# Optimization experiments

Hardware: AMD Instinct MI355X
Metric: run time of the kernel (lower is better)

## Reference

```python
import jax, jax.numpy as jnp
import numpy as np

HEAD_NUM = 16

def setup_inputs() -> dict:
    key = jax.random.key(0)
    k1, k2 = jax.random.split(key)
    bs, seq, d = 2, 2048, 1024
    embeddings = jax.random.normal(k1, (bs, seq, d), dtype=jnp.float32)
    W = jax.random.normal(k2, (d, 3 * d), dtype=jnp.float32) * (1.0 / np.sqrt(d))
    b = jnp.zeros((3 * d,), dtype=jnp.float32)
    return {"embeddings": embeddings, "W": W, "b": b}

def reference(embeddings, W, b):
    bs, seq, d = embeddings.shape
    h = HEAD_NUM
    qkv = embeddings @ W + b                      # [b, s, 3d]
    q, k, v = jnp.split(qkv, 3, axis=-1)          # each [b, s, d]
    hd = d // h
    # Faithful to source: reshape to (bs, seq, head_dim, heads) then permute
    def split_heads(x, head_dim):
        return x.reshape(bs, seq, head_dim, h).transpose(0, 3, 1, 2)  # [b, h, s, hd]
    mq = split_heads(q, hd)
    mk = split_heads(k, hd)
    mv = split_heads(v, hd)
    scale = jnp.sqrt(jnp.asarray(hd, dtype=mq.dtype))
    scores = jnp.einsum('bhqd,bhkd->bhqk', mq, mk) / scale  # [b, h, s, s]
    attn = jax.nn.softmax(scores, axis=-1)
    out = jnp.einsum('bhqk,bhkv->bhqv', attn, mv)            # [b, h, s, hd]
    return out.transpose(0, 2, 1, 3).reshape(bs, seq, -1)    # [b, s, d]
```

## Files before the change

### kernel.cpp

```cpp
#include <hip/hip_runtime.h>
#include <stdint.h>

typedef unsigned short u16;
typedef unsigned int u32;
typedef unsigned int u32x2 __attribute__((ext_vector_type(2)));
typedef float f32x4 __attribute__((ext_vector_type(4)));
typedef __bf16 bf16x8 __attribute__((ext_vector_type(8)));

#define BS 2
#define SEQ 2048
#define DIM 1024
#define NW3 3072
#define NH 16
#define HD 64

#define MFMA_BF16(a, b, c) __builtin_amdgcn_mfma_f32_16x16x32_bf16((a), (b), (c), 0, 0, 0)

#define GLL16(g, l)                                                                \
  __builtin_amdgcn_global_load_lds(                                                \
      (__attribute__((address_space(1))) void*)(void*)(uintptr_t)(g),              \
      (__attribute__((address_space(3))) void*)(l), 16, 0, 0)

__device__ __forceinline__ float fexp2(float x) {
#if defined(__has_builtin)
#if __has_builtin(__builtin_amdgcn_exp2f)
  return __builtin_amdgcn_exp2f(x);
#else
  return exp2f(x);
#endif
#else
  return exp2f(x);
#endif
}

__device__ __forceinline__ u16 f2bf(float x) {
  __bf16 h = (__bf16)x;
  return __builtin_bit_cast(u16, h);
}

#define CSC 0.18033688011112042f

#if defined(__has_builtin)
#if __has_builtin(__builtin_amdgcn_permlane32_swap) && \
    __has_builtin(__builtin_amdgcn_permlane16_swap)
#define HAVE_PLSWAP 1
#endif
#endif

__device__ __forceinline__ uint4 p_transform(u32 pk00, u32 pk01, u32 pk10, u32 pk11,
                                             int sl0, int sl1, bool hi) {
#ifdef HAVE_PLSWAP
  u32x2 s0 = __builtin_amdgcn_permlane32_swap(pk00, pk10, false, false);
  u32x2 s1 = __builtin_amdgcn_permlane32_swap(pk01, pk11, false, false);
  u32x2 t0 = __builtin_amdgcn_permlane16_swap(s0[0], s0[1], false, false);
  u32x2 t1 = __builtin_amdgcn_permlane16_swap(s1[0], s1[1], false, false);
  uint4 wv;
  wv.x = t0[0]; wv.y = t1[0]; wv.z = t0[1]; wv.w = t1[1];
  return wv;
#else
  u32 a0 = __shfl(pk00, sl0), a1 = __shfl(pk01, sl0);
  u32 a2 = __shfl(pk00, sl1), a3 = __shfl(pk01, sl1);
  u32 b0 = __shfl(pk10, sl0), b1 = __shfl(pk11, sl0);
  u32 b2 = __shfl(pk10, sl1), b3 = __shfl(pk11, sl1);
  uint4 wv;
  wv.x = hi ? b0 : a0; wv.y = hi ? b1 : a1;
  wv.z = hi ? b2 : a2; wv.w = hi ? b3 : a3;
  return wv;
#endif
}

__global__ __launch_bounds__(256) void conv_kernel(const float* __restrict__ A,
                                                   u16* __restrict__ O,
                                                   const float* __restrict__ W,
                                                   u16* __restrict__ Wt) {
  if (blockIdx.x < 4096) {
    int i = (blockIdx.x * 256 + threadIdx.x) * 4;
    float4 v = *(const float4*)(A + i);
    union { u16 u[4]; ushort4 v4; } p;
    p.u[0] = f2bf(v.x); p.u[1] = f2bf(v.y); p.u[2] = f2bf(v.z); p.u[3] = f2bf(v.w);
    *(ushort4*)(O + i) = p.v4;
  } else {
    __shared__ __align__(16) u16 lt[64][68];
    int b2 = blockIdx.x - 4096;
    int ktile = b2 / 48, ntile = b2 - ktile * 48;
    int k0 = ktile * 64, n0 = ntile * 64;
    int rowb = threadIdx.x >> 4, c4 = (threadIdx.x & 15) * 4;
#pragma unroll
    for (int rr = 0; rr < 4; ++rr) {
      int row = rowb + rr * 16;
      float4 v = *(const float4*)(W + (size_t)(k0 + row) * NW3 + n0 + c4);
      union { u16 u[4]; uint2 d; } pk;
      pk.u[0] = f2bf(v.x); pk.u[1] = f2bf(v.y); pk.u[2] = f2bf(v.z); pk.u[3] = f2bf(v.w);
      *(uint2*)&lt[row][c4] = pk.d;
    }
    __syncthreads();
    int j = threadIdx.x >> 2, seg = threadIdx.x & 3;
    int n = n0 + j;
    int h = n & 15, hd = (n & 1023) >> 4;
    int np = (n & ~1023) + h * 64 + hd;
    union { u16 u[16]; uint4 q[2]; } o;
#pragma unroll
    for (int idx = 0; idx < 16; ++idx) o.u[idx] = lt[seg * 16 + idx][j];
    u16* dst = Wt + (size_t)np * DIM + k0 + seg * 16;
    *(uint4*)(dst) = o.q[0];
    *(uint4*)(dst + 8) = o.q[1];
  }
}

#define GSTAGE(ADST, BDST, KT)                                                 \
  {                                                                            \
    const int koff = (KT) * 64;                                \
    _Pragma("unroll") for (int r = 0; r < 2; ++r) {                            \
      int l = r * 256 + t;                            \
      int row = l >> 2, pos = l & 3;                                           \
      int kc = pos ^ (row & 3);                                                \
      GLL16(Abase + row * 2048 + koff + kc * 16, (char*)(ADST) + l * 16);      \
      GLL16(Bbase + row * 2048 + koff + kc * 16, (char*)(BDST) + l * 16);      \
    }                                                                          \
  }

#define GCOMPUTE(AT, BT)                                                       \
  {                                                                            \
    bf16x8 af[4], bfr[4];                                                      \
    _Pragma("unroll") for (int mt = 0; mt < 4; ++mt) {                         \
      int row = wm + mt * 16 + c;                                              \
      int kc = quad ^ (row & 3);                                               \
      af[mt] = *(const bf16x8*)((const char*)(AT) + row * 64 + kc * 16);       \
    }                                                                          \
    _Pragma("unroll") for (int nt = 0; nt < 4; ++nt) {                         \
      int row = wn + nt * 16 + c;                                              \
      int kc = quad ^ (row & 3);                                               \
      bfr[nt] = *(const bf16x8*)((const char*)(BT) + row * 64 + kc * 16);      \
    }                                                                          \
    _Pragma("unroll") for (int mt = 0; mt < 4; ++mt)                           \
      _Pragma("unroll") for (int nt = 0; nt < 4; ++nt)                         \
        acc[mt][nt] = MFMA_BF16(af[mt], bfr[nt], acc[mt][nt]);                 \
  }

__global__ __launch_bounds__(256) void gemm_qkv_kernel(
    const u16* __restrict__ Ab, const u16* __restrict__ Bt, const float* __restrict__ bias,
    u16* __restrict__ Q, u16* __restrict__ K, u16* __restrict__ Vt) {
  __shared__ __align__(16) u16 A0[128 * 32];
  __shared__ __align__(16) u16 A1[128 * 32];
  __shared__ __align__(16) u16 A2[128 * 32];
  __shared__ __align__(16) u16 B0[128 * 32];
  __shared__ __align__(16) u16 B1[128 * 32];
  __shared__ __align__(16) u16 B2[128 * 32];
  const int t = threadIdx.x;
  const int lane = t & 63, wave = t >> 6;
  const int c = lane & 15, quad = lane >> 4;
  const int wid = (blockIdx.x & 7) * 96 + (blockIdx.x >> 3);
  const int tm = wid / 24, tn = wid - tm * 24;
  const int wm = (wave >> 1) * 64, wn = (wave & 1) * 64;

  const char* Abase = (const char*)(Ab + (size_t)tm * 128 * DIM);
  const char* Bbase = (const char*)(Bt + (size_t)tn * 128 * DIM);

  f32x4 z = {0.f, 0.f, 0.f, 0.f};
  f32x4 acc[4][4];
#pragma unroll
  for (int i = 0; i < 4; ++i)
#pragma unroll
    for (int j = 0; j < 4; ++j) acc[i][j] = z;

  GSTAGE(A0, B0, 0);
  GSTAGE(A1, B1, 1);
  asm volatile("s_waitcnt vmcnt(4)" ::: "memory");
  __builtin_amdgcn_s_barrier();
  __builtin_amdgcn_sched_barrier(0);

  const u16 *pa = A0, *pb = B0;
  const u16 *qa = A1, *qb = B1;
  const u16 *ra = A2, *rb = B2;
#pragma unroll 1
  for (int kt = 0; kt < 32; ++kt) {
    if (kt + 2 < 32) GSTAGE(ra, rb, kt + 2);
    GCOMPUTE(pa, pb);
    if (kt + 2 < 32) {
      asm volatile("s_waitcnt vmcnt(4)" ::: "memory");
    } else {
      asm volatile("s_waitcnt vmcnt(0)" ::: "memory");
    }
    __builtin_amdgcn_s_barrier();
    __builtin_amdgcn_sched_barrier(0);
    const u16* ta = pa; pa = qa; qa = ra; ra = ta;
    const u16* tb = pb; pb = qb; qb = rb; rb = tb;
  }

#pragma unroll
  for (int nt = 0; nt < 4; ++nt) {
    int np = tn * 128 + wn + nt * 16 + c;
    int which = np >> 10;
    int rem = np & 1023;
    int h = rem >> 6, hd = rem & 63;
    float bv = bias[(np & ~1023) + hd * 16 + h];
    float sc = (which == 0) ? CSC : 1.0f;
    float bvs = bv * sc;
#pragma unroll
    for (int mt = 0; mt < 4; ++mt) {
      int mbase = tm * 128 + wm + mt * 16 + quad * 4;
      int bI = mbase >> 11;
      int s0 = mbase & 2047;
      if (which == 2) {
        union { u16 u[4]; uint2 v; } p;
#pragma unroll
        for (int r = 0; r < 4; ++r) p.u[r] = f2bf(acc[mt][nt][r] + bv);
        *(uint2*)(Vt + ((size_t)(bI * NH + h) * HD + hd) * SEQ + s0) = p.v;
      } else {
        u16* dst = (which == 0) ? Q : K;
#pragma unroll
        for (int r = 0; r < 4; ++r)
          dst[((size_t)(bI * NH + h) * SEQ + (s0 + r)) * HD + hd] =
              f2bf(acc[mt][nt][r] * sc + bvs);
      }
    }
  }
}

#define STAGE_KV(KDST, VDST, KTILE)                                            \
  {                                                                            \
    const char* Ktb = Kb + (size_t)(KTILE) * 8192;        \
    const char* Vtb = Vb + (size_t)(KTILE) * 128;         \
    _Pragma("unroll") for (int r = 0; r < 2; ++r) {                            \
      int l = r * 256 + t;                                                     \
      int row = l >> 3, pos = l & 7;                                           \
      int kc = pos ^ (row & 7);                                                \
      GLL16(Ktb + row * 128 + kc * 16, (char*)(KDST) + l * 16);                \
      GLL16(Vtb + row * 4096 + kc * 16, (char*)(VDST) + l * 16);               \
    }                                                                          \
  }

#define COMPUTE_TILE(KT, VT)                                                   \
  {                                                                            \
    f32x4 sT[2][2]; \
    sT[0][0] = z; sT[0][1] = z; sT[1][0] = z; sT[1][1] = z;                    \
    __builtin_amdgcn_s_setprio(1);                                             \
    _Pragma("unroll") for (int mt2 = 0; mt2 < 2; ++mt2) {                      \
      _Pragma("unroll") for (int ks = 0; ks < 2; ++ks) {                       \
        int row = ws * 32 + mt2 * 16 + c;                                      \
        int kc = (ks * 4 + quad) ^ (row & 7);                                  \
        bf16x8 kf = *(const bf16x8*)((const char*)(KT) + row * 128 + kc * 16); \
        sT[mt2][0] = MFMA_BF16(kf, qf[0][ks], sT[mt2][0]);                     \
        sT[mt2][1] = MFMA_BF16(kf, qf[1][ks], sT[mt2][1]);                     \
      }                                                                        \
    }                                                                          \
    __builtin_amdgcn_s_setprio(0);                                             \
    bf16x8 pf[2];                                                              \
    _Pragma("unroll") for (int nt = 0; nt < 2; ++nt) {                         \
      u32 pk[2][2];                                                            \
      _Pragma("unroll") for (int mt2 = 0; mt2 < 2; ++mt2) {                    \
        float p0 = fexp2(sT[mt2][nt][0]);                                      \
        float p1 = fexp2(sT[mt2][nt][1]);                                      \
        float p2 = fexp2(sT[mt2][nt][2]);                                      \
        float p3 = fexp2(sT[mt2][nt][3]);                                      \
        pk[mt2][0] = (u32)f2bf(p0) | ((u32)f2bf(p1) << 16);                    \
        pk[mt2][1] = (u32)f2bf(p2) | ((u32)f2bf(p3) << 16);                    \
      }                                                                        \
      uint4 wv = p_transform(pk[0][0], pk[0][1], pk[1][0], pk[1][1],           \
                             sl0, sl1, hi);                                    \
      pf[nt] = __builtin_bit_cast(bf16x8, wv);                                 \
    }                                                                          \
    __builtin_amdgcn_s_setprio(1);                                             \
    _Pragma("unroll") for (int mt = 0; mt < 4; ++mt) {                         \
      int row = mt * 16 + c;                                                   \
      int kc = vq ^ (row & 7);                                                 \
      bf16x8 vf = *(const bf16x8*)((const char*)(VT) + row * 128 + kc * 16);   \
      accO[mt][0] = MFMA_BF16(vf, pf[0], accO[mt][0]);                         \
      accO[mt][1] = MFMA_BF16(vf, pf[1], accO[mt][1]);                         \
    }                                                                          \
    acc_l[0] = MFMA_BF16(ones, pf[0], acc_l[0]);   \
    acc_l[1] = MFMA_BF16(ones, pf[1], acc_l[1]);                               \
    __builtin_amdgcn_s_setprio(0);                                             \
  }

__global__ __launch_bounds__(256, 4) void attn_kernel(
    const u16* __restrict__ Q, const u16* __restrict__ K,
    const u16* __restrict__ Vt, float* __restrict__ Out) {
  __shared__ __align__(16) u16 Ka[64 * 64];
  __shared__ __align__(16) u16 Kb2[64 * 64];
  __shared__ __align__(16) u16 Va[64 * 64];
  __shared__ __align__(16) u16 Vb2[64 * 64];
  const int t = threadIdx.x;
  const int lane = t & 63, wave = t >> 6;
  const int c = lane & 15, quad = lane >> 4;
  const int wq = wave & 1, ws = wave >> 1;
  const int p = blockIdx.x;
  const int xcd = p & 7, slot = p >> 3;
  const int bh = xcd + ((slot >> 5) << 3);
  const int qt = slot & 31;
  const int h = bh & 15, b = bh >> 4;

  const u16* Qb = Q + ((size_t)bh * SEQ + qt * 64) * HD;
  const char* Kb = (const char*)(K + (size_t)bh * SEQ * HD);
  const char* Vb = (const char*)(Vt + (size_t)bh * HD * SEQ);

#pragma unroll
  for (int r = 0; r < 2; ++r) {
    int l = r * 256 + t;
    int row = l >> 3, pos = l & 7;
    int kc = pos ^ (row & 7);
    GLL16((const char*)Qb + row * 128 + kc * 16, (char*)Ka + l * 16);
  }
  __syncthreads();
  bf16x8 qf[2][2];
#pragma unroll
  for (int nt = 0; nt < 2; ++nt)
#pragma unroll
    for (int ks = 0; ks < 2; ++ks) {
      int row = wq * 32 + nt * 16 + c;
      int kc = (ks * 4 + quad) ^ (row & 7);
      qf[nt][ks] = *(const bf16x8*)((const char*)Ka + row * 128 + kc * 16);
    }
  __syncthreads();

  f32x4 z = {0.f, 0.f, 0.f, 0.f};
  f32x4 accO[4][2];
#pragma unroll
  for (int i = 0; i < 4; ++i) { accO[i][0] = z; accO[i][1] = z; }
  f32x4 acc_l[2] = {z, z};
  const uint4 onesw = {0x3F803F80u, 0x3F803F80u, 0x3F803F80u, 0x3F803F80u};
  const bf16x8 ones = __builtin_bit_cast(bf16x8, onesw);

  const int sl0 = c + 16 * ((quad & 1) * 2);
  const int sl1 = sl0 + 16;
  const bool hi = quad >= 2;
  const int vq = ws * 4 + quad;

  STAGE_KV(Ka, Va, 0);
  __syncthreads();

  for (int kt = 0; kt < 32; kt += 2) {
    STAGE_KV(Kb2, Vb2, kt + 1);
    COMPUTE_TILE(Ka, Va);
    __syncthreads();
    if (kt + 2 < 32) STAGE_KV(Ka, Va, kt + 2);
    COMPUTE_TILE(Kb2, Vb2);
    __syncthreads();
  }

  float sm[2];
  sm[0] = acc_l[0][0];
  sm[1] = acc_l[1][0];
  if (ws == 1) {
    float* fb = (float*)(wq ? (void*)Kb2 : (void*)Ka);
#pragma unroll
    for (int mt = 0; mt < 4; ++mt)
#pragma unroll
      for (int nt = 0; nt < 2; ++nt)
        *(f32x4*)(fb + (mt * 2 + nt) * 256 + lane * 4) = accO[mt][nt];
    float* lb = (float*)Va + wq * 128;
    lb[lane * 2] = sm[0];
    lb[lane * 2 + 1] = sm[1];
  }
  __syncthreads();
  if (ws == 0) {
    const float* fb = (const float*)(wq ? (void*)Kb2 : (void*)Ka);
#pragma unroll
    for (int mt = 0; mt < 4; ++mt)
#pragma unroll
      for (int nt = 0; nt < 2; ++nt)
        accO[mt][nt] += *(const f32x4*)(fb + (mt * 2 + nt) * 256 + lane * 4);
    const float* lb = (const float*)Va + wq * 128;
    float inv0 = 1.f / (sm[0] + lb[lane * 2]);
    float inv1 = 1.f / (sm[1] + lb[lane * 2 + 1]);
    int s0 = qt * 64 + wq * 32 + c;
#pragma unroll
    for (int mt = 0; mt < 4; ++mt) {
#pragma unroll
      for (int nt = 0; nt < 2; ++nt) {
        float inv = nt ? inv1 : inv0;
        float4 o;
        o.x = accO[mt][nt][0] * inv;
        o.y = accO[mt][nt][1] * inv;
        o.z = accO[mt][nt][2] * inv;
        o.w = accO[mt][nt][3] * inv;
        size_t off = ((size_t)(b * SEQ + s0 + nt * 16)) * DIM + h * HD + mt * 16 + quad * 4;
        *(float4*)(Out + off) = o;
      }
    }
  }
}

extern "C" void kernel_launch(void* const* d_in, const int* in_sizes, int n_in,
                              void* d_out, int out_size, void* d_ws, size_t ws_size,
                              hipStream_t stream) {
  (void)in_sizes; (void)n_in; (void)out_size; (void)ws_size;
  const float* emb = (const float*)d_in[0];
  const float* W = (const float*)d_in[1];
  const float* bias = (const float*)d_in[2];
  float* out = (float*)d_out;
  char* ws = (char*)d_ws;
  u16* Ab = (u16*)ws;
  u16* Wt = (u16*)(ws + 8388608);
  u16* Qd = (u16*)(ws + 14680064);
  u16* Kd = (u16*)(ws + 23068672);
  u16* Vd = (u16*)(ws + 31457280);

  conv_kernel<<<4864, 256, 0, stream>>>(emb, Ab, W, Wt);
  gemm_qkv_kernel<<<768, 256, 0, stream>>>(Ab, Wt, bias, Qd, Kd, Vd);
  attn_kernel<<<1024, 256, 0, stream>>>(Qd, Kd, Vd, out);
}
```

Baseline: 160.2 us.

## Double attention query tile to 128 rows per 512-thread block

The attention kernel now runs 8 waves per block covering 128 query rows instead of 4 waves covering 64, so each staged K/V tile in shared memory is shared by twice as many query rows. This halves the global K/V traffic and the number of blocks (512 instead of 1024). Each thread now issues one async load per tile instead of two, and a separate shared buffer is added for the row-sum reduction. The trade-offs are fewer blocks to fill the GPU, less parallelism in the load phase, and larger per-block barriers.

```diff
diff --git a/kernel.cpp b/kernel.cpp
--- a/kernel.cpp
+++ b/kernel.cpp
@@ -221,13 +221,11 @@
   {                                                                            \
     const char* Ktb = Kb + (size_t)(KTILE) * 8192;        \
     const char* Vtb = Vb + (size_t)(KTILE) * 128;         \
-    _Pragma("unroll") for (int r = 0; r < 2; ++r) {                            \
-      int l = r * 256 + t;                                                     \
-      int row = l >> 3, pos = l & 7;                                           \
-      int kc = pos ^ (row & 7);                                                \
-      GLL16(Ktb + row * 128 + kc * 16, (char*)(KDST) + l * 16);                \
-      GLL16(Vtb + row * 4096 + kc * 16, (char*)(VDST) + l * 16);               \
-    }                                                                          \
+    int l = t;                             \
+    int row = l >> 3, pos = l & 7;                                             \
+    int kc = pos ^ (row & 7);                                                  \
+    GLL16(Ktb + row * 128 + kc * 16, (char*)(KDST) + l * 16);                  \
+    GLL16(Vtb + row * 4096 + kc * 16, (char*)(VDST) + l * 16);                 \
   }
 
 #define COMPUTE_TILE(KT, VT)                                                   \
@@ -273,33 +271,34 @@
     __builtin_amdgcn_s_setprio(0);                                             \
   }
 
-__global__ __launch_bounds__(256, 4) void attn_kernel(
+__global__ __launch_bounds__(512, 4) void attn_kernel(
     const u16* __restrict__ Q, const u16* __restrict__ K,
     const u16* __restrict__ Vt, float* __restrict__ Out) {
   __shared__ __align__(16) u16 Ka[64 * 64];
   __shared__ __align__(16) u16 Kb2[64 * 64];
   __shared__ __align__(16) u16 Va[64 * 64];
   __shared__ __align__(16) u16 Vb2[64 * 64];
+  __shared__ float lred[512];
   const int t = threadIdx.x;
   const int lane = t & 63, wave = t >> 6;
   const int c = lane & 15, quad = lane >> 4;
-  const int wq = wave & 1, ws = wave >> 1;
+  const int wq2 = wave & 3, ws = wave >> 2;
   const int p = blockIdx.x;
   const int xcd = p & 7, slot = p >> 3;
-  const int bh = xcd + ((slot >> 5) << 3);
-  const int qt = slot & 31;
+  const int bh = xcd + ((slot >> 4) << 3);
+  const int qtp = slot & 15;
   const int h = bh & 15, b = bh >> 4;
 
-  const u16* Qb = Q + ((size_t)bh * SEQ + qt * 64) * HD;
+  const u16* Qb = Q + ((size_t)bh * SEQ + qtp * 128) * HD;
   const char* Kb = (const char*)(K + (size_t)bh * SEQ * HD);
   const char* Vb = (const char*)(Vt + (size_t)bh * HD * SEQ);
 
-#pragma unroll
-  for (int r = 0; r < 2; ++r) {
-    int l = r * 256 + t;
+  {
+    int l = t;
     int row = l >> 3, pos = l & 7;
     int kc = pos ^ (row & 7);
     GLL16((const char*)Qb + row * 128 + kc * 16, (char*)Ka + l * 16);
+    GLL16((const char*)Qb + 8192 + row * 128 + kc * 16, (char*)Va + l * 16);
   }
   __syncthreads();
   bf16x8 qf[2][2];
@@ -307,9 +306,10 @@
   for (int nt = 0; nt < 2; ++nt)
 #pragma unroll
     for (int ks = 0; ks < 2; ++ks) {
-      int row = wq * 32 + nt * 16 + c;
+      int row = (wq2 & 1) * 32 + nt * 16 + c;
       int kc = (ks * 4 + quad) ^ (row & 7);
-      qf[nt][ks] = *(const bf16x8*)((const char*)Ka + row * 128 + kc * 16);
+      const char* qbuf = (wq2 >> 1) ? (const char*)Va : (const char*)Ka;
+      qf[nt][ks] = *(const bf16x8*)(qbuf + row * 128 + kc * 16);
     }
   __syncthreads();
 
@@ -341,29 +341,27 @@
   float sm[2];
   sm[0] = acc_l[0][0];
   sm[1] = acc_l[1][0];
+  float* fb = (float*)((wq2 & 2) ? ((wq2 & 1) ? (void*)Vb2 : (void*)Va)
+                                 : ((wq2 & 1) ? (void*)Kb2 : (void*)Ka));
   if (ws == 1) {
-    float* fb = (float*)(wq ? (void*)Kb2 : (void*)Ka);
 #pragma unroll
     for (int mt = 0; mt < 4; ++mt)
 #pragma unroll
       for (int nt = 0; nt < 2; ++nt)
         *(f32x4*)(fb + (mt * 2 + nt) * 256 + lane * 4) = accO[mt][nt];
-    float* lb = (float*)Va + wq * 128;
-    lb[lane * 2] = sm[0];
-    lb[lane * 2 + 1] = sm[1];
+    lred[wq2 * 128 + lane * 2] = sm[0];
+    lred[wq2 * 128 + lane * 2 + 1] = sm[1];
   }
   __syncthreads();
   if (ws == 0) {
-    const float* fb = (const float*)(wq ? (void*)Kb2 : (void*)Ka);
 #pragma unroll
     for (int mt = 0; mt < 4; ++mt)
 #pragma unroll
       for (int nt = 0; nt < 2; ++nt)
         accO[mt][nt] += *(const f32x4*)(fb + (mt * 2 + nt) * 256 + lane * 4);
-    const float* lb = (const float*)Va + wq * 128;
-    float inv0 = 1.f / (sm[0] + lb[lane * 2]);
-    float inv1 = 1.f / (sm[1] + lb[lane * 2 + 1]);
-    int s0 = qt * 64 + wq * 32 + c;
+    float inv0 = 1.f / (sm[0] + lred[wq2 * 128 + lane * 2]);
+    float inv1 = 1.f / (sm[1] + lred[wq2 * 128 + lane * 2 + 1]);
+    int s0 = qtp * 128 + wq2 * 32 + c;
 #pragma unroll
     for (int mt = 0; mt < 4; ++mt) {
 #pragma unroll
@@ -398,5 +396,5 @@
 
   conv_kernel<<<4864, 256, 0, stream>>>(emb, Ab, W, Wt);
   gemm_qkv_kernel<<<768, 256, 0, stream>>>(Ab, Wt, bias, Qd, Kd, Vd);
-  attn_kernel<<<1024, 256, 0, stream>>>(Qd, Kd, Vd, out);
-}
+  attn_kernel<<<512, 512, 0, stream>>>(Qd, Kd, Vd, out);
+}
```

Result: faster. 155.1 us (median of 4 runs) (-3.2%).
